# Kernel tuning notes

Measured on AMD Instinct MI355X. Metric: run time of the kernel, lower is better.

Reference implementation:

```python
import jax, jax.numpy as jnp
import numpy as np

N, E, FEAT, C, H, D, L, T, MS, MD, NC = 20000, 320000, 128, 256, 8, 32, 5, 64, 10, 128, 2
NEG_SLOPE = 0.2


def setup_inputs() -> dict:
    key = jax.random.key(0)
    ks = jax.random.split(key, 20)
    g = lambda k, shape, fan: jax.random.normal(k, shape, jnp.float32) / np.sqrt(fan)
    return {
        "x_initial_nodes": jax.random.normal(ks[0], (N, FEAT), jnp.float32),
        "edge_index": jax.random.randint(ks[1], (2, E), 0, N, jnp.int32),
        "time_embedding": jax.random.normal(ks[2], (N, T), jnp.float32),
        "Wi": g(ks[3], (FEAT, C), FEAT),
        "bi": jnp.zeros((C,), jnp.float32),
        "Wg": g(ks[4], (L, C, C), C),          # GAT projection per layer
        "a_src": g(ks[5], (L, H, D), D),        # attention vectors
        "a_dst": g(ks[6], (L, H, D), D),
        "Wt": g(ks[7], (L, T, C), T),           # time-embedding fusion
        "Wq": g(ks[8], (L, C, C), C),           # memory cross-attention
        "Wk": g(ks[9], (L, MD, C), MD),
        "Wv": g(ks[10], (L, MD, C), MD),
        "global_memory": jax.random.normal(ks[11], (MS, MD), jnp.float32),
        "Wc": g(ks[12], (C + MD, NC), C + MD),
        "bc": jnp.zeros((NC,), jnp.float32),
    }


def _stm_layer(x, src, dst, t_proj, mem, Wg, a_s, a_d, Wq, Wk, Wv):
    # GAT-style message passing with time fusion
    h = ((x + t_proj) @ Wg).reshape(N, H, D)                      # [N,H,D]
    e_src = jnp.einsum('nhd,hd->nh', h, a_s)                      # [N,H]
    e_dst = jnp.einsum('nhd,hd->nh', h, a_d)
    logits = jax.nn.leaky_relu(e_src[src] + e_dst[dst], NEG_SLOPE)  # [E,H]
    m = jax.ops.segment_max(logits, dst, num_segments=N)
    m = jnp.where(jnp.isfinite(m), m, 0.0)                        # empty segments
    ex = jnp.exp(logits - m[dst])
    denom = jax.ops.segment_sum(ex, dst, num_segments=N)
    alpha = ex / (denom[dst] + 1e-16)                             # [E,H]
    msg = jax.ops.segment_sum(alpha[:, :, None] * h[src], dst, num_segments=N)
    node = jax.nn.relu(msg.reshape(N, C))
    # cross-attention to global memory bank
    q = node @ Wq                                                  # [N,C]
    k = mem @ Wk                                                   # [MS,C]
    v = mem @ Wv                                                   # [MS,C]
    attn = jax.nn.softmax(q @ k.T / np.sqrt(C), axis=-1)           # [N,MS]
    return jax.nn.relu(node + attn @ v + x)                        # residual


def reference(x_initial_nodes, edge_index, time_embedding, Wi, bi, Wg, a_src,
              a_dst, Wt, Wq, Wk, Wv, global_memory, Wc, bc):
    src, dst = edge_index[0], edge_index[1]
    node = jax.nn.relu(x_initial_nodes @ Wi + bi)                  # [N,C]
    for l in range(L):
        t_proj = time_embedding @ Wt[l]                            # [N,C]
        node = _stm_layer(node, src, dst, t_proj, global_memory,
                          Wg[l], a_src[l], a_dst[l], Wq[l], Wk[l], Wv[l])
    pooled = jnp.mean(node, axis=0)                                # [C]
    mem_pooled = jnp.mean(global_memory, axis=0)                   # [MD]
    final = jnp.concatenate([pooled, mem_pooled], axis=-1)         # [C+MD]
    return final @ Wc + bc                                         # [NC]
```

## Files before the change

kernel.cpp:

```cpp
#include <hip/hip_runtime.h>
#include <hip/hip_bf16.h>

#define N_NODES 20000
#define E_EDGES 320000
#define FEAT 128
#define CDIM 256
#define NHEAD 8
#define HDIM 32
#define NLAYER 5
#define TDIM 64
#define MSLOT 10
#define MDIM 128
#define NCLS 2

typedef unsigned short ushort_t;
typedef unsigned char uchar_t;
typedef short short8 __attribute__((ext_vector_type(8)));
typedef float floatx4 __attribute__((ext_vector_type(4)));
typedef float floatx2 __attribute__((ext_vector_type(2)));

__device__ __forceinline__ ushort_t f2bf(float f) {
    union { float f; unsigned int u; } t; t.f = f;
    unsigned int r = (t.u + 0x7FFF + ((t.u >> 16) & 1)) >> 16;
    return (ushort_t)r;
}
__device__ __forceinline__ float bf2f(ushort_t u) {
    union { float f; unsigned int u; } t; t.u = ((unsigned int)u) << 16;
    return t.f;
}

__global__ __launch_bounds__(256) void gemm_mfma(
    const ushort_t* __restrict__ A1, int lda1, int K1,
    const ushort_t* __restrict__ A2, int lda2, int Ktot,
    const ushort_t* __restrict__ Bt,
    const float* __restrict__ bias,
    ushort_t* Cbf, int doRelu)
{
    __shared__ __align__(16) ushort_t smemA[32 * 32];
    __shared__ __align__(16) ushort_t smemB[128 * 32];
    int tid = threadIdx.x;
    int lane = tid & 63, wid = tid >> 6;
    int li = lane & 15, lq = lane >> 4;
    int row0 = blockIdx.y * 32;
    int col0 = blockIdx.x * 128;

    floatx4 acc[2][2];
#pragma unroll
    for (int a = 0; a < 2; a++)
#pragma unroll
        for (int b = 0; b < 2; b++) acc[a][b] = {0.f, 0.f, 0.f, 0.f};

    int ar = tid >> 2, ac = tid & 3;
    int agc = (ac - (ar >> 1)) & 3;

    for (int k0 = 0; k0 < Ktot; k0 += 32) {
        __syncthreads();
        const ushort_t* Ab; int lda;
        if (k0 < K1) { Ab = A1 + k0; lda = lda1; }
        else         { Ab = A2 + (k0 - K1); lda = lda2; }
        if (wid < 2) {
            const void* g = (const void*)(Ab + (size_t)(row0 + ar) * lda + agc * 8);
            __builtin_amdgcn_global_load_lds(
                (const __attribute__((address_space(1))) void*)g,
                (__attribute__((address_space(3))) void*)&smemA[wid * 512], 16, 0, 0);
        }
#pragma unroll
        for (int j = 0; j < 2; j++) {
            int slot = j * 256 + tid;
            int n = slot >> 2, c = slot & 3;
            int gc = (c - (n >> 1)) & 3;
            const void* g = (const void*)(Bt + (size_t)(col0 + n) * Ktot + k0 + gc * 8);
            __builtin_amdgcn_global_load_lds(
                (const __attribute__((address_space(1))) void*)g,
                (__attribute__((address_space(3))) void*)&smemB[(j * 256 + wid * 64) * 8], 16, 0, 0);
        }
        __syncthreads();

        short8 af[2], bfr[2];
#pragma unroll
        for (int mt = 0; mt < 2; mt++) {
            int m = mt * 16 + li;
            int sw = (lq + (m >> 1)) & 3;
            af[mt] = *(const short8*)&smemA[m * 32 + sw * 8];
        }
#pragma unroll
        for (int nt = 0; nt < 2; nt++) {
            int nl = wid * 32 + nt * 16 + li;
            int sw = (lq + (nl >> 1)) & 3;
            bfr[nt] = *(const short8*)&smemB[nl * 32 + sw * 8];
        }
#pragma unroll
        for (int mt = 0; mt < 2; mt++)
#pragma unroll
            for (int nt = 0; nt < 2; nt++)
                acc[mt][nt] = __builtin_amdgcn_mfma_f32_16x16x32_bf16(af[mt], bfr[nt], acc[mt][nt], 0, 0, 0);
    }

#pragma unroll
    for (int mt = 0; mt < 2; mt++) {
        int row = row0 + mt * 16 + lq * 4;
#pragma unroll
        for (int nt = 0; nt < 2; nt++) {
            int col = col0 + wid * 32 + nt * 16 + li;
            float bv = bias ? bias[col] : 0.f;
#pragma unroll
            for (int r = 0; r < 4; r++) {
                float v = acc[mt][nt][r] + bv;
                if (doRelu) v = fmaxf(v, 0.f);
                Cbf[(size_t)(row + r) * CDIM + col] = f2bf(v);
            }
        }
    }
}

__global__ __launch_bounds__(256) void gemm_h(
    const ushort_t* __restrict__ A1, int lda1, int K1,
    const ushort_t* __restrict__ A2, int lda2, int Ktot,
    const ushort_t* __restrict__ Bt,
    const float* __restrict__ a_s, const float* __restrict__ a_d,
    uchar_t* __restrict__ Cf8,
    float* __restrict__ esrc, float* __restrict__ edst)
{
    __shared__ __align__(16) ushort_t smemA[32 * 32];
    __shared__ __align__(16) ushort_t smemB[128 * 32];
    int tid = threadIdx.x;
    int lane = tid & 63, wid = tid >> 6;
    int li = lane & 15, lq = lane >> 4;
    int row0 = blockIdx.y * 32;
    int col0 = blockIdx.x * 128;

    floatx4 acc[2][2];
#pragma unroll
    for (int a = 0; a < 2; a++)
#pragma unroll
        for (int b = 0; b < 2; b++) acc[a][b] = {0.f, 0.f, 0.f, 0.f};

    int ar = tid >> 2, ac = tid & 3;
    int agc = (ac - (ar >> 1)) & 3;

    for (int k0 = 0; k0 < Ktot; k0 += 32) {
        __syncthreads();
        const ushort_t* Ab; int lda;
        if (k0 < K1) { Ab = A1 + k0; lda = lda1; }
        else         { Ab = A2 + (k0 - K1); lda = lda2; }
        if (wid < 2) {
            const void* g = (const void*)(Ab + (size_t)(row0 + ar) * lda + agc * 8);
            __builtin_amdgcn_global_load_lds(
                (const __attribute__((address_space(1))) void*)g,
                (__attribute__((address_space(3))) void*)&smemA[wid * 512], 16, 0, 0);
        }
#pragma unroll
        for (int j = 0; j < 2; j++) {
            int slot = j * 256 + tid;
            int n = slot >> 2, c = slot & 3;
            int gc = (c - (n >> 1)) & 3;
            const void* g = (const void*)(Bt + (size_t)(col0 + n) * Ktot + k0 + gc * 8);
            __builtin_amdgcn_global_load_lds(
                (const __attribute__((address_space(1))) void*)g,
                (__attribute__((address_space(3))) void*)&smemB[(j * 256 + wid * 64) * 8], 16, 0, 0);
        }
        __syncthreads();

        short8 af[2], bfr[2];
#pragma unroll
        for (int mt = 0; mt < 2; mt++) {
            int m = mt * 16 + li;
            int sw = (lq + (m >> 1)) & 3;
            af[mt] = *(const short8*)&smemA[m * 32 + sw * 8];
        }
#pragma unroll
        for (int nt = 0; nt < 2; nt++) {
            int nl = wid * 32 + nt * 16 + li;
            int sw = (lq + (nl >> 1)) & 3;
            bfr[nt] = *(const short8*)&smemB[nl * 32 + sw * 8];
        }
#pragma unroll
        for (int mt = 0; mt < 2; mt++)
#pragma unroll
            for (int nt = 0; nt < 2; nt++)
                acc[mt][nt] = __builtin_amdgcn_mfma_f32_16x16x32_bf16(af[mt], bfr[nt], acc[mt][nt], 0, 0, 0);
    }

    int hd = blockIdx.x * 4 + wid;
    int cbase = col0 + wid * 32 + li;
    float as0 = a_s[cbase];
    float as1 = a_s[cbase + 16];
    float ad0 = a_d[cbase];
    float ad1 = a_d[cbase + 16];

#pragma unroll
    for (int mt = 0; mt < 2; mt++) {
        int row = row0 + mt * 16 + lq * 4;
#pragma unroll
        for (int r = 0; r < 4; r++) {
            float v0 = acc[mt][0][r];
            float v1 = acc[mt][1][r];
            unsigned int pk = __builtin_amdgcn_cvt_pk_fp8_f32(v0, v1, 0, false);
            Cf8[(size_t)(row + r) * CDIM + cbase]      = (uchar_t)(pk & 0xff);
            Cf8[(size_t)(row + r) * CDIM + cbase + 16] = (uchar_t)((pk >> 8) & 0xff);
            float ps = v0 * as0 + v1 * as1;
            float pd = v0 * ad0 + v1 * ad1;
#pragma unroll
            for (int d = 1; d < 16; d <<= 1) {
                ps += __shfl_xor(ps, d);
                pd += __shfl_xor(pd, d);
            }
            if (li == 0) {
                esrc[(size_t)(row + r) * NHEAD + hd] = ps;
                edst[(size_t)(row + r) * NHEAD + hd] = pd;
            }
        }
    }
}

__global__ __launch_bounds__(256) void gemm64(
    const float* __restrict__ A, const float* __restrict__ A2,
    const float* __restrict__ B, const float* __restrict__ bias,
    float* __restrict__ C, int M, int K, int Nf, int doRelu,
    int sA, int sB, int sC)
{
    __shared__ float As[16][64];
    __shared__ float Bs[16][64];
    A += (size_t)blockIdx.z * sA;
    B += (size_t)blockIdx.z * sB;
    C += (size_t)blockIdx.z * sC;
    int tid = threadIdx.x;
    int tx = tid & 15, ty = tid >> 4;
    int row0 = blockIdx.y * 64, col0 = blockIdx.x * 64;
    int ar = tid >> 2;
    int ac = (tid & 3) * 4;

    float acc[4][4] = {};

    for (int k0 = 0; k0 < K; k0 += 16) {
        int arow = row0 + ar;
        float4 av = make_float4(0.f, 0.f, 0.f, 0.f);
        if (arow < M) {
            av = *(const float4*)(A + (size_t)arow * K + k0 + ac);
            if (A2) {
                float4 a2 = *(const float4*)(A2 + (size_t)arow * K + k0 + ac);
                av.x += a2.x; av.y += a2.y; av.z += a2.z; av.w += a2.w;
            }
        }
        As[ac + 0][ar] = av.x;
        As[ac + 1][ar] = av.y;
        As[ac + 2][ar] = av.z;
        As[ac + 3][ar] = av.w;
        float4 bv = *(const float4*)(B + (size_t)(k0 + (tid >> 4)) * Nf + col0 + (tid & 15) * 4);
        *(float4*)&Bs[tid >> 4][(tid & 15) * 4] = bv;
        __syncthreads();
#pragma unroll
        for (int kk = 0; kk < 16; kk++) {
            float4 a = *(const float4*)&As[kk][ty * 4];
            float4 b = *(const float4*)&Bs[kk][tx * 4];
            acc[0][0] += a.x * b.x; acc[0][1] += a.x * b.y; acc[0][2] += a.x * b.z; acc[0][3] += a.x * b.w;
            acc[1][0] += a.y * b.x; acc[1][1] += a.y * b.y; acc[1][2] += a.y * b.z; acc[1][3] += a.y * b.w;
            acc[2][0] += a.z * b.x; acc[2][1] += a.z * b.y; acc[2][2] += a.z * b.z; acc[2][3] += a.z * b.w;
            acc[3][0] += a.w * b.x; acc[3][1] += a.w * b.y; acc[3][2] += a.w * b.z; acc[3][3] += a.w * b.w;
        }
        __syncthreads();
    }

    float4 bv = make_float4(0.f, 0.f, 0.f, 0.f);
    if (bias) bv = *(const float4*)(bias + col0 + tx * 4);
#pragma unroll
    for (int i = 0; i < 4; i++) {
        int r = row0 + ty * 4 + i;
        if (r < M) {
            float4 o;
            o.x = acc[i][0] + bv.x;
            o.y = acc[i][1] + bv.y;
            o.z = acc[i][2] + bv.z;
            o.w = acc[i][3] + bv.w;
            if (doRelu) {
                o.x = fmaxf(o.x, 0.f); o.y = fmaxf(o.y, 0.f);
                o.z = fmaxf(o.z, 0.f); o.w = fmaxf(o.w, 0.f);
            }
            *(float4*)(C + (size_t)r * Nf + col0 + tx * 4) = o;
        }
    }
}

__global__ void cvt_bf16(const float* __restrict__ in, ushort_t* __restrict__ out, int n)
{
    int i = blockIdx.x * blockDim.x + threadIdx.x;
    if (i < n) out[i] = f2bf(in[i]);
}

__global__ __launch_bounds__(256) void transpose_cast(
    const float* __restrict__ in, int K, int Nn,
    ushort_t* __restrict__ out, int ostride, int koff,
    int inBatchStride, int outBatchStride)
{
    __shared__ float tile[32][33];
    in  += (size_t)blockIdx.z * inBatchStride;
    out += (size_t)blockIdx.z * outBatchStride;
    int k0 = blockIdx.y * 32, n0 = blockIdx.x * 32;
    int tx = threadIdx.x & 31, ty = threadIdx.x >> 5;
#pragma unroll
    for (int j = 0; j < 4; j++)
        tile[ty + j * 8][tx] = in[(size_t)(k0 + ty + j * 8) * Nn + n0 + tx];
    __syncthreads();
#pragma unroll
    for (int j = 0; j < 4; j++) {
        int n = n0 + ty + j * 8;
        out[(size_t)n * ostride + koff + k0 + tx] = f2bf(tile[tx][ty + j * 8]);
    }
}

__global__ __launch_bounds__(256) void wqk_build(
    const float* __restrict__ Wq, const float* __restrict__ kbufs,
    float* __restrict__ wqk)
{
    int j = blockIdx.x, l = blockIdx.y;
    int d = threadIdx.x;
    __shared__ float kk[CDIM];
    kk[d] = kbufs[((size_t)l * MSLOT + j) * CDIM + d];
    __syncthreads();
    const float* wrow = Wq + ((size_t)l * CDIM + d) * CDIM;
    float acc = 0.f;
#pragma unroll 4
    for (int c = 0; c < CDIM; c++) acc += wrow[c] * kk[c];
    wqk[((size_t)l * MSLOT + j) * CDIM + d] = acc * 0.0625f;
}

__global__ void count_deg(const int* __restrict__ dst, int* __restrict__ deg, int ne)
{
    int e = blockIdx.x * blockDim.x + threadIdx.x;
    if (e < ne) atomicAdd(&deg[dst[e]], 1);
}

__global__ __launch_bounds__(1024) void scan_kernel(const int* __restrict__ deg,
                                                    int* __restrict__ offs, int n)
{
    __shared__ int swt[16];
    int tid = threadIdx.x, lane = tid & 63, wid = tid >> 6;
    int base = tid * 20;
    int v[20];
    int s = 0;
#pragma unroll
    for (int i = 0; i < 20; i++) {
        int d = (base + i < n) ? deg[base + i] : 0;
        v[i] = d; s += d;
    }
    int x = s;
#pragma unroll
    for (int d = 1; d < 64; d <<= 1) {
        int t = __shfl_up(x, d);
        if (lane >= d) x += t;
    }
    if (lane == 63) swt[wid] = x;
    __syncthreads();
    if (wid == 0) {
        int w = (lane < 16) ? swt[lane] : 0;
#pragma unroll
        for (int d = 1; d < 16; d <<= 1) {
            int t = __shfl_up(w, d);
            if (lane >= d) w += t;
        }
        if (lane < 16) swt[lane] = w;
    }
    __syncthreads();
    int wbase = (wid == 0) ? 0 : swt[wid - 1];
    int run = wbase + x - s;
#pragma unroll
    for (int i = 0; i < 20; i++) {
        if (base + i < n) offs[base + i] = run;
        run += v[i];
    }
}

__global__ void fill_csr(const int* __restrict__ src, const int* __restrict__ dst,
                         const int* __restrict__ offs, int* __restrict__ cursor,
                         int* __restrict__ csr_src, int ne)
{
    int e = blockIdx.x * blockDim.x + threadIdx.x;
    if (e < ne) {
        int d = dst[e];
        int p = atomicAdd(&cursor[d], 1);
        csr_src[offs[d] + p] = src[e];
    }
}

__global__ __launch_bounds__(256) void gat_agg_fused(
    const uchar_t* __restrict__ h, const float* __restrict__ esrc, const float* __restrict__ edst,
    const int* __restrict__ offs, const int* __restrict__ deg, const int* __restrict__ csr_src,
    const float* __restrict__ wqk, const float* __restrict__ vbuf,
    const ushort_t* __restrict__ node_in,
    ushort_t* __restrict__ node_out, int n)
{
    int tid = threadIdx.x;
    int lane = tid & 63;
    int wslot = tid >> 6;
    int node = blockIdx.x * 4 + wslot;
    int start = offs[node], cnt = deg[node];
    int chead = lane >> 3;

    float4 gat4;
    if (cnt <= 64) {
        int eh = lane >> 3, hh = lane & 7;
        float edl = edst[(size_t)node * NHEAD + hh];
        int sl = (lane < cnt) ? csr_src[start + lane] : 0;
        int nit = (cnt + 7) >> 3;
        float lg[8], w8[8];
        float m = -3.0e38f;
#pragma unroll
        for (int it = 0; it < 8; it++) {
            float v = -3.0e38f;
            if (it < nit) {
                int e = it * 8 + eh;
                int se = __shfl(sl, e);
                if (e < cnt) {
                    float t = esrc[(size_t)se * NHEAD + hh] + edl;
                    v = t > 0.f ? t : 0.2f * t;
                }
            }
            lg[it] = v;
            m = fmaxf(m, v);
        }
        m = fmaxf(m, __shfl_xor(m, 8));
        m = fmaxf(m, __shfl_xor(m, 16));
        m = fmaxf(m, __shfl_xor(m, 32));
        float den = 0.f;
#pragma unroll
        for (int it = 0; it < 8; it++) {
            float w = 0.f;
            if (it < nit) {
                int e = it * 8 + eh;
                if (e < cnt) w = __expf(lg[it] - m);
            }
            w8[it] = w;
            den += w;
        }
        den += __shfl_xor(den, 8);
        den += __shfl_xor(den, 16);
        den += __shfl_xor(den, 32);
        float inv = 1.f / (den + 1e-16f);
        float invc = __shfl(inv, chead);

        float4 acc = make_float4(0.f, 0.f, 0.f, 0.f);
#pragma unroll
        for (int rr = 0; rr < 8; rr++) {
            if (rr < nit) {
                int sv[8]; float av[8];
#pragma unroll
                for (int k = 0; k < 8; k++) {
                    sv[k] = __shfl(sl, rr * 8 + k);
                    av[k] = __shfl(w8[rr], (k << 3) | chead);
                }
                unsigned int hw[8];
#pragma unroll
                for (int k = 0; k < 8; k++)
                    hw[k] = *(const unsigned int*)(h + (size_t)sv[k] * CDIM + lane * 4);
#pragma unroll
                for (int k = 0; k < 8; k++) {
                    floatx2 lo = __builtin_amdgcn_cvt_pk_f32_fp8((int)hw[k], false);
                    floatx2 hi = __builtin_amdgcn_cvt_pk_f32_fp8((int)hw[k], true);
                    acc.x += av[k] * lo.x;
                    acc.y += av[k] * lo.y;
                    acc.z += av[k] * hi.x;
                    acc.w += av[k] * hi.y;
                }
            }
        }
        gat4.x = fmaxf(acc.x * invc, 0.f);
        gat4.y = fmaxf(acc.y * invc, 0.f);
        gat4.z = fmaxf(acc.z * invc, 0.f);
        gat4.w = fmaxf(acc.w * invc, 0.f);
    } else {
        int hh = lane & 7;
        float edl = edst[(size_t)node * NHEAD + hh];
        float m = -3.0e38f;
        int i8 = lane >> 3;
        for (int i = 0; i < cnt; i += 8) {
            int ii = i + i8;
            if (ii < cnt) {
                int s = csr_src[start + ii];
                float lgv = esrc[(size_t)s * NHEAD + hh] + edl;
                lgv = lgv > 0.f ? lgv : 0.2f * lgv;
                m = fmaxf(m, lgv);
            }
        }
        m = fmaxf(m, __shfl_xor(m, 8));
        m = fmaxf(m, __shfl_xor(m, 16));
        m = fmaxf(m, __shfl_xor(m, 32));
        float4 acc = make_float4(0.f, 0.f, 0.f, 0.f);
        float den = 0.f;
        for (int i = 0; i < cnt; i++) {
            int s = csr_src[start + i];
            float lgv = esrc[(size_t)s * NHEAD + hh] + edl;
            lgv = lgv > 0.f ? lgv : 0.2f * lgv;
            float w = __expf(lgv - m);
            den += w;
            float wc = __shfl(w, chead);
            unsigned int hwv = *(const unsigned int*)(h + (size_t)s * CDIM + lane * 4);
            floatx2 lo = __builtin_amdgcn_cvt_pk_f32_fp8((int)hwv, false);
            floatx2 hi = __builtin_amdgcn_cvt_pk_f32_fp8((int)hwv, true);
            acc.x += wc * lo.x; acc.y += wc * lo.y;
            acc.z += wc * hi.x; acc.w += wc * hi.y;
        }
        float dc = __shfl(den, chead) + 1e-16f;
        float inv = 1.f / dc;
        gat4.x = fmaxf(acc.x * inv, 0.f);
        gat4.y = fmaxf(acc.y * inv, 0.f);
        gat4.z = fmaxf(acc.z * inv, 0.f);
        gat4.w = fmaxf(acc.w * inv, 0.f);
    }

    float s[MSLOT];
#pragma unroll
    for (int j = 0; j < MSLOT; j++) {
        float4 w4 = *(const float4*)(wqk + j * CDIM + lane * 4);
        s[j] = gat4.x * w4.x + gat4.y * w4.y + gat4.z * w4.z + gat4.w * w4.w;
    }
#pragma unroll
    for (int d = 1; d < 64; d <<= 1) {
#pragma unroll
        for (int j = 0; j < MSLOT; j++) s[j] += __shfl_xor(s[j], d);
    }
    float m = s[0];
#pragma unroll
    for (int j = 1; j < MSLOT; j++) m = fmaxf(m, s[j]);
    float sum = 0.f;
#pragma unroll
    for (int j = 0; j < MSLOT; j++) { s[j] = __expf(s[j] - m); sum += s[j]; }
    float inv = 1.f / sum;

    ushort4 c4 = *(const ushort4*)(node_in + (size_t)node * CDIM + lane * 4);
    float4 o;
    o.x = gat4.x + bf2f(c4.x); o.y = gat4.y + bf2f(c4.y);
    o.z = gat4.z + bf2f(c4.z); o.w = gat4.w + bf2f(c4.w);
#pragma unroll
    for (int j = 0; j < MSLOT; j++) {
        float p = s[j] * inv;
        float4 v4 = *(const float4*)(vbuf + j * CDIM + lane * 4);
        o.x += p * v4.x; o.y += p * v4.y; o.z += p * v4.z; o.w += p * v4.w;
    }
    o.x = fmaxf(o.x, 0.f); o.y = fmaxf(o.y, 0.f); o.z = fmaxf(o.z, 0.f); o.w = fmaxf(o.w, 0.f);
    ushort4 ob;
    ob.x = f2bf(o.x); ob.y = f2bf(o.y); ob.z = f2bf(o.z); ob.w = f2bf(o.w);
    *(ushort4*)(node_out + (size_t)node * CDIM + lane * 4) = ob;
}

__global__ void col_sum(const ushort_t* __restrict__ node, float* __restrict__ pooled, int n)
{
    float acc = 0.f;
    int c = threadIdx.x;
    for (int r = blockIdx.x; r < n; r += gridDim.x) acc += bf2f(node[(size_t)r * CDIM + c]);
    atomicAdd(&pooled[c], acc);
}

__global__ void finalize(const float* __restrict__ pooled, const float* __restrict__ mem,
                         const float* __restrict__ Wc, const float* __restrict__ bc,
                         float* __restrict__ out)
{
    int lane = threadIdx.x;
    float a0 = 0.f, a1 = 0.f;
    for (int i = lane; i < CDIM + MDIM; i += 64) {
        float f;
        if (i < CDIM) {
            f = pooled[i] * (1.0f / (float)N_NODES);
        } else {
            float s = 0.f;
            for (int r = 0; r < MSLOT; r++) s += mem[r * MDIM + (i - CDIM)];
            f = s * (1.0f / (float)MSLOT);
        }
        a0 += f * Wc[i * NCLS + 0];
        a1 += f * Wc[i * NCLS + 1];
    }
#pragma unroll
    for (int d = 1; d < 64; d <<= 1) { a0 += __shfl_xor(a0, d); a1 += __shfl_xor(a1, d); }
    if (lane == 0) { out[0] = a0 + bc[0]; out[1] = a1 + bc[1]; }
}

extern "C" void kernel_launch(void* const* d_in, const int* in_sizes, int n_in,
                              void* d_out, int out_size, void* d_ws, size_t ws_size,
                              hipStream_t stream)
{
    const float* x    = (const float*)d_in[0];
    const int*   ei   = (const int*)d_in[1];
    const float* temb = (const float*)d_in[2];
    const float* Wi   = (const float*)d_in[3];
    const float* bi   = (const float*)d_in[4];
    const float* Wg   = (const float*)d_in[5];
    const float* a_s  = (const float*)d_in[6];
    const float* a_d  = (const float*)d_in[7];
    const float* Wt   = (const float*)d_in[8];
    const float* Wq   = (const float*)d_in[9];
    const float* Wk   = (const float*)d_in[10];
    const float* Wv   = (const float*)d_in[11];
    const float* mem  = (const float*)d_in[12];
    const float* Wc   = (const float*)d_in[13];
    const float* bc   = (const float*)d_in[14];
    float* out = (float*)d_out;
    char* ws = (char*)d_ws;

    const size_t NCB_BYTES = (size_t)N_NODES * CDIM * 2;
    size_t off = 0;
    ushort_t* nodeA  = (ushort_t*)(ws + off); off += NCB_BYTES;
    ushort_t* nodeB  = (ushort_t*)(ws + off); off += NCB_BYTES;
    uchar_t*  hf8    = (uchar_t*)(ws + off);  off += (size_t)N_NODES * CDIM;
    ushort_t* xbf    = (ushort_t*)(ws + off); off += (size_t)N_NODES * FEAT * 2;
    ushort_t* tembbf = (ushort_t*)(ws + off); off += (size_t)N_NODES * TDIM * 2;
    float* esrc   = (float*)(ws + off); off += (size_t)N_NODES * NHEAD * 4;
    float* edst   = (float*)(ws + off); off += (size_t)N_NODES * NHEAD * 4;
    float* kbufs  = (float*)(ws + off); off += (size_t)NLAYER * MSLOT * CDIM * 4;
    float* vbufs  = (float*)(ws + off); off += (size_t)NLAYER * MSLOT * CDIM * 4;
    float* wqkL   = (float*)(ws + off); off += (size_t)NLAYER * MSLOT * CDIM * 4;
    float* Wtp    = (float*)(ws + off); off += (size_t)NLAYER * TDIM * CDIM * 4;
    ushort_t* Bt_i = (ushort_t*)(ws + off); off += (size_t)CDIM * FEAT * 2;
    ushort_t* Bt_h = (ushort_t*)(ws + off); off += (size_t)NLAYER * CDIM * (CDIM + TDIM) * 2;
    size_t zero_base = off;
    float* pooled = (float*)(ws + off); off += CDIM * 4;
    int* deg      = (int*)(ws + off);   off += N_NODES * 4;
    int* cursor   = (int*)(ws + off);   off += N_NODES * 4;
    size_t zero_len = off - zero_base;
    int* offs     = (int*)(ws + off);   off += (N_NODES + 4) * 4;
    int* csr_src  = (int*)(ws + off);   off += (size_t)E_EDGES * 4;

    const int* srcIdx = ei;
    const int* dstIdx = ei + E_EDGES;

    hipMemsetAsync(ws + zero_base, 0, zero_len, stream);

    cvt_bf16<<<(N_NODES * FEAT + 255) / 256, 256, 0, stream>>>(x, xbf, N_NODES * FEAT);
    cvt_bf16<<<(N_NODES * TDIM + 255) / 256, 256, 0, stream>>>(temb, tembbf, N_NODES * TDIM);
    gemm64<<<dim3(4, 1, NLAYER), 256, 0, stream>>>(Wt, nullptr, Wg, nullptr, Wtp,
        TDIM, CDIM, CDIM, 0, TDIM * CDIM, CDIM * CDIM, TDIM * CDIM);
    transpose_cast<<<dim3(CDIM / 32, FEAT / 32, 1), 256, 0, stream>>>(
        Wi, FEAT, CDIM, Bt_i, FEAT, 0, 0, 0);
    transpose_cast<<<dim3(CDIM / 32, CDIM / 32, NLAYER), 256, 0, stream>>>(
        Wg, CDIM, CDIM, Bt_h, CDIM + TDIM, 0, CDIM * CDIM, CDIM * (CDIM + TDIM));
    transpose_cast<<<dim3(CDIM / 32, TDIM / 32, NLAYER), 256, 0, stream>>>(
        Wtp, TDIM, CDIM, Bt_h, CDIM + TDIM, CDIM, TDIM * CDIM, CDIM * (CDIM + TDIM));
    gemm64<<<dim3(4, 1, NLAYER), 256, 0, stream>>>(mem, nullptr, Wk, nullptr, kbufs,
        MSLOT, MDIM, CDIM, 0, 0, MDIM * CDIM, MSLOT * CDIM);
    gemm64<<<dim3(4, 1, NLAYER), 256, 0, stream>>>(mem, nullptr, Wv, nullptr, vbufs,
        MSLOT, MDIM, CDIM, 0, 0, MDIM * CDIM, MSLOT * CDIM);
    wqk_build<<<dim3(MSLOT, NLAYER), 256, 0, stream>>>(Wq, kbufs, wqkL);

    count_deg<<<(E_EDGES + 255) / 256, 256, 0, stream>>>(dstIdx, deg, E_EDGES);
    scan_kernel<<<1, 1024, 0, stream>>>(deg, offs, N_NODES);
    fill_csr<<<(E_EDGES + 255) / 256, 256, 0, stream>>>(srcIdx, dstIdx, offs, cursor, csr_src, E_EDGES);

    dim3 mfmaGrid(2, N_NODES / 32);
    int nodeBlocks = N_NODES / 4;

    gemm_mfma<<<mfmaGrid, 256, 0, stream>>>(xbf, FEAT, FEAT, nullptr, 0, FEAT,
                                            Bt_i, bi, nodeA, 1);

    ushort_t* cur = nodeA;
    ushort_t* alt = nodeB;
    for (int l = 0; l < NLAYER; l++) {
        gemm_h<<<mfmaGrid, 256, 0, stream>>>(cur, CDIM, CDIM, tembbf, TDIM, CDIM + TDIM,
                                             Bt_h + (size_t)l * CDIM * (CDIM + TDIM),
                                             a_s + (size_t)l * CDIM, a_d + (size_t)l * CDIM,
                                             hf8, esrc, edst);
        gat_agg_fused<<<nodeBlocks, 256, 0, stream>>>(hf8, esrc, edst, offs, deg, csr_src,
                                                      wqkL + (size_t)l * MSLOT * CDIM,
                                                      vbufs + (size_t)l * MSLOT * CDIM,
                                                      cur, alt, N_NODES);
        ushort_t* t = cur; cur = alt; alt = t;
    }

    col_sum<<<128, 256, 0, stream>>>(cur, pooled, N_NODES);
    finalize<<<1, 64, 0, stream>>>(pooled, mem, Wc, bc, out);
}
```

Measured before the change: 479.2 us.

## Deepen GEMM K-tile, prefetch neighbor features in GAT aggregation, vectorize col_sum

The two MFMA GEMM kernels now stage a 64-wide K slice per iteration instead of 32, with a wider 8-chunk swizzle and two MFMA sub-steps per tile. This halves the number of barrier pairs and global-to-LDS rounds. The GAT aggregation kernel issues the gathers of up to 32 source-node fp8 rows, and the residual row load, before the softmax computation so their latency overlaps that math. Edges beyond 32 fall back to the old loop. col_sum is rewritten to read four bf16 values per thread across four rows per block, which raises register pressure in the aggregation kernel and LDS use in the GEMMs.

```diff
diff --git a/kernel.cpp b/kernel.cpp
--- a/kernel.cpp
+++ b/kernel.cpp
@@ -36,8 +36,8 @@
     const float* __restrict__ bias,
     ushort_t* Cbf, int doRelu)
 {
-    __shared__ __align__(16) ushort_t smemA[32 * 32];
-    __shared__ __align__(16) ushort_t smemB[128 * 32];
+    __shared__ __align__(16) ushort_t smemA[32 * 64];
+    __shared__ __align__(16) ushort_t smemB[128 * 64];
     int tid = threadIdx.x;
     int lane = tid & 63, wid = tid >> 6;
     int li = lane & 15, lq = lane >> 4;
@@ -50,25 +50,25 @@
 #pragma unroll
         for (int b = 0; b < 2; b++) acc[a][b] = {0.f, 0.f, 0.f, 0.f};
 
-    int ar = tid >> 2, ac = tid & 3;
-    int agc = (ac - (ar >> 1)) & 3;
-
-    for (int k0 = 0; k0 < Ktot; k0 += 32) {
+    int ar = tid >> 3, ac = tid & 7;
+    int agc = (ac - (ar >> 1)) & 7;
+
+    for (int k0 = 0; k0 < Ktot; k0 += 64) {
         __syncthreads();
         const ushort_t* Ab; int lda;
         if (k0 < K1) { Ab = A1 + k0; lda = lda1; }
         else         { Ab = A2 + (k0 - K1); lda = lda2; }
-        if (wid < 2) {
+        {
             const void* g = (const void*)(Ab + (size_t)(row0 + ar) * lda + agc * 8);
             __builtin_amdgcn_global_load_lds(
                 (const __attribute__((address_space(1))) void*)g,
                 (__attribute__((address_space(3))) void*)&smemA[wid * 512], 16, 0, 0);
         }
 #pragma unroll
-        for (int j = 0; j < 2; j++) {
+        for (int j = 0; j < 4; j++) {
             int slot = j * 256 + tid;
-            int n = slot >> 2, c = slot & 3;
-            int gc = (c - (n >> 1)) & 3;
+            int n = slot >> 3, c = slot & 7;
+            int gc = (c - (n >> 1)) & 7;
             const void* g = (const void*)(Bt + (size_t)(col0 + n) * Ktot + k0 + gc * 8);
             __builtin_amdgcn_global_load_lds(
                 (const __attribute__((address_space(1))) void*)g,
@@ -76,24 +76,27 @@
         }
         __syncthreads();
 
-        short8 af[2], bfr[2];
-#pragma unroll
-        for (int mt = 0; mt < 2; mt++) {
-            int m = mt * 16 + li;
-            int sw = (lq + (m >> 1)) & 3;
-            af[mt] = *(const short8*)&smemA[m * 32 + sw * 8];
-        }
-#pragma unroll
-        for (int nt = 0; nt < 2; nt++) {
-            int nl = wid * 32 + nt * 16 + li;
-            int sw = (lq + (nl >> 1)) & 3;
-            bfr[nt] = *(const short8*)&smemB[nl * 32 + sw * 8];
-        }
-#pragma unroll
-        for (int mt = 0; mt < 2; mt++)
-#pragma unroll
-            for (int nt = 0; nt < 2; nt++)
-                acc[mt][nt] = __builtin_amdgcn_mfma_f32_16x16x32_bf16(af[mt], bfr[nt], acc[mt][nt], 0, 0, 0);
+#pragma unroll
+        for (int ks = 0; ks < 2; ks++) {
+            short8 af[2], bfr[2];
+#pragma unroll
+            for (int mt = 0; mt < 2; mt++) {
+                int m = mt * 16 + li;
+                int sw = ((ks * 4 + lq) + (m >> 1)) & 7;
+                af[mt] = *(const short8*)&smemA[m * 64 + sw * 8];
+            }
+#pragma unroll
+            for (int nt = 0; nt < 2; nt++) {
+                int nl = wid * 32 + nt * 16 + li;
+                int sw = ((ks * 4 + lq) + (nl >> 1)) & 7;
+                bfr[nt] = *(const short8*)&smemB[nl * 64 + sw * 8];
+            }
+#pragma unroll
+            for (int mt = 0; mt < 2; mt++)
+#pragma unroll
+                for (int nt = 0; nt < 2; nt++)
+                    acc[mt][nt] = __builtin_amdgcn_mfma_f32_16x16x32_bf16(af[mt], bfr[nt], acc[mt][nt], 0, 0, 0);
+        }
     }
 
 #pragma unroll
@@ -121,8 +124,8 @@
     uchar_t* __restrict__ Cf8,
     float* __restrict__ esrc, float* __restrict__ edst)
 {
-    __shared__ __align__(16) ushort_t smemA[32 * 32];
-    __shared__ __align__(16) ushort_t smemB[128 * 32];
+    __shared__ __align__(16) ushort_t smemA[32 * 64];
+    __shared__ __align__(16) ushort_t smemB[128 * 64];
     int tid = threadIdx.x;
     int lane = tid & 63, wid = tid >> 6;
     int li = lane & 15, lq = lane >> 4;
@@ -135,25 +138,25 @@
 #pragma unroll
         for (int b = 0; b < 2; b++) acc[a][b] = {0.f, 0.f, 0.f, 0.f};
 
-    int ar = tid >> 2, ac = tid & 3;
-    int agc = (ac - (ar >> 1)) & 3;
-
-    for (int k0 = 0; k0 < Ktot; k0 += 32) {
+    int ar = tid >> 3, ac = tid & 7;
+    int agc = (ac - (ar >> 1)) & 7;
+
+    for (int k0 = 0; k0 < Ktot; k0 += 64) {
         __syncthreads();
         const ushort_t* Ab; int lda;
         if (k0 < K1) { Ab = A1 + k0; lda = lda1; }
         else         { Ab = A2 + (k0 - K1); lda = lda2; }
-        if (wid < 2) {
+        {
             const void* g = (const void*)(Ab + (size_t)(row0 + ar) * lda + agc * 8);
             __builtin_amdgcn_global_load_lds(
                 (const __attribute__((address_space(1))) void*)g,
                 (__attribute__((address_space(3))) void*)&smemA[wid * 512], 16, 0, 0);
         }
 #pragma unroll
-        for (int j = 0; j < 2; j++) {
+        for (int j = 0; j < 4; j++) {
             int slot = j * 256 + tid;
-            int n = slot >> 2, c = slot & 3;
-            int gc = (c - (n >> 1)) & 3;
+            int n = slot >> 3, c = slot & 7;
+            int gc = (c - (n >> 1)) & 7;
             const void* g = (const void*)(Bt + (size_t)(col0 + n) * Ktot + k0 + gc * 8);
             __builtin_amdgcn_global_load_lds(
                 (const __attribute__((address_space(1))) void*)g,
@@ -161,24 +164,27 @@
         }
         __syncthreads();
 
-        short8 af[2], bfr[2];
-#pragma unroll
-        for (int mt = 0; mt < 2; mt++) {
-            int m = mt * 16 + li;
-            int sw = (lq + (m >> 1)) & 3;
-            af[mt] = *(const short8*)&smemA[m * 32 + sw * 8];
-        }
-#pragma unroll
-        for (int nt = 0; nt < 2; nt++) {
-            int nl = wid * 32 + nt * 16 + li;
-            int sw = (lq + (nl >> 1)) & 3;
-            bfr[nt] = *(const short8*)&smemB[nl * 32 + sw * 8];
-        }
-#pragma unroll
-        for (int mt = 0; mt < 2; mt++)
-#pragma unroll
-            for (int nt = 0; nt < 2; nt++)
-                acc[mt][nt] = __builtin_amdgcn_mfma_f32_16x16x32_bf16(af[mt], bfr[nt], acc[mt][nt], 0, 0, 0);
+#pragma unroll
+        for (int ks = 0; ks < 2; ks++) {
+            short8 af[2], bfr[2];
+#pragma unroll
+            for (int mt = 0; mt < 2; mt++) {
+                int m = mt * 16 + li;
+                int sw = ((ks * 4 + lq) + (m >> 1)) & 7;
+                af[mt] = *(const short8*)&smemA[m * 64 + sw * 8];
+            }
+#pragma unroll
+            for (int nt = 0; nt < 2; nt++) {
+                int nl = wid * 32 + nt * 16 + li;
+                int sw = ((ks * 4 + lq) + (nl >> 1)) & 7;
+                bfr[nt] = *(const short8*)&smemB[nl * 64 + sw * 8];
+            }
+#pragma unroll
+            for (int mt = 0; mt < 2; mt++)
+#pragma unroll
+                for (int nt = 0; nt < 2; nt++)
+                    acc[mt][nt] = __builtin_amdgcn_mfma_f32_16x16x32_bf16(af[mt], bfr[nt], acc[mt][nt], 0, 0, 0);
+        }
     }
 
     int hd = blockIdx.x * 4 + wid;
@@ -396,12 +402,28 @@
     int start = offs[node], cnt = deg[node];
     int chead = lane >> 3;
 
+    ushort4 c4 = *(const ushort4*)(node_in + (size_t)node * CDIM + lane * 4);
+
     float4 gat4;
     if (cnt <= 64) {
         int eh = lane >> 3, hh = lane & 7;
         float edl = edst[(size_t)node * NHEAD + hh];
         int sl = (lane < cnt) ? csr_src[start + lane] : 0;
         int nit = (cnt + 7) >> 3;
+        int npf = nit < 4 ? nit : 4;
+
+        unsigned int hw[4][8];
+#pragma unroll
+        for (int rr = 0; rr < 4; rr++) {
+            if (rr < npf) {
+#pragma unroll
+                for (int k = 0; k < 8; k++) {
+                    int sv = __shfl(sl, rr * 8 + k);
+                    hw[rr][k] = *(const unsigned int*)(h + (size_t)sv * CDIM + lane * 4);
+                }
+            }
+        }
+
         float lg[8], w8[8];
         float m = -3.0e38f;
 #pragma unroll
@@ -440,27 +462,39 @@
 
         float4 acc = make_float4(0.f, 0.f, 0.f, 0.f);
 #pragma unroll
-        for (int rr = 0; rr < 8; rr++) {
-            if (rr < nit) {
-                int sv[8]; float av[8];
+        for (int rr = 0; rr < 4; rr++) {
+            if (rr < npf) {
+                float av[8];
+#pragma unroll
+                for (int k = 0; k < 8; k++)
+                    av[k] = __shfl(w8[rr], (k << 3) | chead);
 #pragma unroll
                 for (int k = 0; k < 8; k++) {
-                    sv[k] = __shfl(sl, rr * 8 + k);
-                    av[k] = __shfl(w8[rr], (k << 3) | chead);
-                }
-                unsigned int hw[8];
-#pragma unroll
-                for (int k = 0; k < 8; k++)
-                    hw[k] = *(const unsigned int*)(h + (size_t)sv[k] * CDIM + lane * 4);
-#pragma unroll
-                for (int k = 0; k < 8; k++) {
-                    floatx2 lo = __builtin_amdgcn_cvt_pk_f32_fp8((int)hw[k], false);
-                    floatx2 hi = __builtin_amdgcn_cvt_pk_f32_fp8((int)hw[k], true);
+                    floatx2 lo = __builtin_amdgcn_cvt_pk_f32_fp8((int)hw[rr][k], false);
+                    floatx2 hi = __builtin_amdgcn_cvt_pk_f32_fp8((int)hw[rr][k], true);
                     acc.x += av[k] * lo.x;
                     acc.y += av[k] * lo.y;
                     acc.z += av[k] * hi.x;
                     acc.w += av[k] * hi.y;
                 }
+            }
+        }
+        for (int rr = 4; rr < nit; rr++) {
+            int sv[8]; float av[8];
+#pragma unroll
+            for (int k = 0; k < 8; k++) {
+                sv[k] = __shfl(sl, rr * 8 + k);
+                av[k] = __shfl(w8[rr], (k << 3) | chead);
+            }
+#pragma unroll
+            for (int k = 0; k < 8; k++) {
+                unsigned int hwv = *(const unsigned int*)(h + (size_t)sv[k] * CDIM + lane * 4);
+                floatx2 lo = __builtin_amdgcn_cvt_pk_f32_fp8((int)hwv, false);
+                floatx2 hi = __builtin_amdgcn_cvt_pk_f32_fp8((int)hwv, true);
+                acc.x += av[k] * lo.x;
+                acc.y += av[k] * lo.y;
+                acc.z += av[k] * hi.x;
+                acc.w += av[k] * hi.y;
             }
         }
         gat4.x = fmaxf(acc.x * invc, 0.f);
@@ -526,7 +560,6 @@
     for (int j = 0; j < MSLOT; j++) { s[j] = __expf(s[j] - m); sum += s[j]; }
     float inv = 1.f / sum;
 
-    ushort4 c4 = *(const ushort4*)(node_in + (size_t)node * CDIM + lane * 4);
     float4 o;
     o.x = gat4.x + bf2f(c4.x); o.y = gat4.y + bf2f(c4.y);
     o.z = gat4.z + bf2f(c4.z); o.w = gat4.w + bf2f(c4.w);
@@ -542,12 +575,20 @@
     *(ushort4*)(node_out + (size_t)node * CDIM + lane * 4) = ob;
 }
 
-__global__ void col_sum(const ushort_t* __restrict__ node, float* __restrict__ pooled, int n)
-{
-    float acc = 0.f;
-    int c = threadIdx.x;
-    for (int r = blockIdx.x; r < n; r += gridDim.x) acc += bf2f(node[(size_t)r * CDIM + c]);
-    atomicAdd(&pooled[c], acc);
+__global__ __launch_bounds__(256) void col_sum(const ushort_t* __restrict__ node,
+                                               float* __restrict__ pooled, int n)
+{
+    int cg = (threadIdx.x & 63) * 4;
+    int rofs = threadIdx.x >> 6;
+    float4 acc = make_float4(0.f, 0.f, 0.f, 0.f);
+    for (int r = blockIdx.x * 4 + rofs; r < n; r += gridDim.x * 4) {
+        ushort4 v = *(const ushort4*)(node + (size_t)r * CDIM + cg);
+        acc.x += bf2f(v.x); acc.y += bf2f(v.y); acc.z += bf2f(v.z); acc.w += bf2f(v.w);
+    }
+    atomicAdd(&pooled[cg + 0], acc.x);
+    atomicAdd(&pooled[cg + 1], acc.y);
+    atomicAdd(&pooled[cg + 2], acc.z);
+    atomicAdd(&pooled[cg + 3], acc.w);
 }
 
 __global__ void finalize(const float* __restrict__ pooled, const float* __restrict__ mem,
```

Measured after the change: 526.6 us. +9.9%, slower.
